# Kernel tuning notes

Measured on AMD Instinct MI355X. Metric: run time of the kernel, lower is better.

The kernel has to match this reference:

```python
import jax, jax.numpy as jnp
import numpy as np

B, T, D = 2, 2048, 2048
H, HKV, RD = 16, 4, 64
DH = D // H          # 128
REP = H // HKV       # 4
NEG = -1e30


def _apply_rope(x, cos, sin, rd):
    # x: (B, h, T, Dh); cos/sin: (T, rd//2) broadcast over (B, h)
    xr, xp = x[..., :rd], x[..., rd:]
    x1, x2 = xr[..., ::2], xr[..., 1::2]
    rot = jnp.stack([x1 * cos - x2 * sin, x1 * sin + x2 * cos], axis=-1)
    rot = rot.reshape(x1.shape[:-1] + (rd,))
    return jnp.concatenate([rot, xp], axis=-1)


def setup_inputs() -> dict:
    key = jax.random.key(0)
    ks = jax.random.split(key, 6)
    x = jax.random.normal(ks[0], (B, T, D), dtype=jnp.float32)
    # rotary tables for the first RD dims (RD//2 frequency pairs)
    inv_freq = 1.0 / (10000.0 ** (np.arange(RD // 2, dtype=np.float32) / (RD // 2)))
    ang = np.arange(T, dtype=np.float32)[:, None] * inv_freq[None, :]  # (T, RD//2)
    cos = jnp.asarray(np.cos(ang), dtype=jnp.float32)
    sin = jnp.asarray(np.sin(ang), dtype=jnp.float32)
    s = 0.02
    Wq = jax.random.normal(ks[1], (H * DH, D), dtype=jnp.float32) * s
    Wk = jax.random.normal(ks[2], (HKV * DH, D), dtype=jnp.float32) * s
    Wv = jax.random.normal(ks[3], (HKV * DH, D), dtype=jnp.float32) * s
    Wo = jax.random.normal(ks[4], (D, D), dtype=jnp.float32) * s
    temp = jnp.full((H,), 1.0 / np.sqrt(DH), dtype=jnp.float32)
    return {"x": x, "cos": cos, "sin": sin, "Wq": Wq, "Wk": Wk, "Wv": Wv, "Wo": Wo, "temp": temp}


def reference(x, cos, sin, Wq, Wk, Wv, Wo, temp):
    Bt, Tt, _ = x.shape
    q = (x @ Wq.T).reshape(Bt, Tt, H, DH).transpose(0, 2, 1, 3)    # (B,H,T,Dh)
    k = (x @ Wk.T).reshape(Bt, Tt, HKV, DH).transpose(0, 2, 1, 3)  # (B,Hkv,T,Dh)
    v = (x @ Wv.T).reshape(Bt, Tt, HKV, DH).transpose(0, 2, 1, 3)
    k = jnp.repeat(k, REP, axis=1)  # GQA repeat_interleave -> (B,H,T,Dh)
    v = jnp.repeat(v, REP, axis=1)
    q = _apply_rope(q, cos, sin, RD)
    k = _apply_rope(k, cos, sin, RD)
    q = q * temp[None, :, None, None]
    # SDPA causal, with default 1/sqrt(Dh) scale on top of learned temp
    scores = jnp.einsum("bhqd,bhkd->bhqk", q, k) / np.sqrt(DH)
    causal = jnp.tril(jnp.ones((Tt, Tt), dtype=bool))
    scores = jnp.where(causal[None, None], scores, NEG)
    attn = jax.nn.softmax(scores, axis=-1)
    out = jnp.einsum("bhqk,bhkd->bhqd", attn, v)  # (B,H,T,Dh)
    out = out.transpose(0, 2, 1, 3).reshape(Bt, Tt, H * DH)
    return out @ Wo.T
```

## Files before the change

### kernel.cpp

```cpp
#include <hip/hip_runtime.h>
#include <hip/hip_bf16.h>
#include <math.h>

#define B_   2
#define T_   2048
#define D_   2048
#define H_   16
#define HKV_ 4
#define DH_  128
#define RD_  64
#define KD_  (HKV_ * DH_)
#define SQKV 3072
#define VOFF 2560

typedef __attribute__((ext_vector_type(8))) short  short8;
typedef __attribute__((ext_vector_type(4))) short  short4v;
typedef __attribute__((ext_vector_type(4))) float  floatx4;

__device__ __forceinline__ void async16(const __hip_bfloat16* g, __hip_bfloat16* l) {
  __builtin_amdgcn_global_load_lds(
      (const __attribute__((address_space(1))) void*)g,
      (__attribute__((address_space(3))) void*)l, 16, 0, 0);
}

__device__ __forceinline__ short bf16b(float x) {
  union { __hip_bfloat16 h; short s; } u;
  u.h = __float2bfloat16(x);
  return u.s;
}

struct ConvArgs {
  const float* src[5];
  __hip_bfloat16* dst[5];
  int n[5];
};

__global__ __launch_bounds__(256) void conv_bf16(ConvArgs a) {
  const int arr = blockIdx.y;
  const int i = (blockIdx.x * 256 + threadIdx.x) * 8;
  if (i >= a.n[arr]) return;
  const float4 f1 = *(const float4*)(a.src[arr] + i);
  const float4 f2 = *(const float4*)(a.src[arr] + i + 4);
  union { short8 v; __hip_bfloat16 h[8]; } o;
  o.h[0] = __float2bfloat16(f1.x); o.h[1] = __float2bfloat16(f1.y);
  o.h[2] = __float2bfloat16(f1.z); o.h[3] = __float2bfloat16(f1.w);
  o.h[4] = __float2bfloat16(f2.x); o.h[5] = __float2bfloat16(f2.y);
  o.h[6] = __float2bfloat16(f2.z); o.h[7] = __float2bfloat16(f2.w);
  *(short8*)(a.dst[arr] + i) = o.v;
}

template <int MODE>
__global__ __launch_bounds__(512, 1) void gemm_192(const __hip_bfloat16* __restrict__ A,
                                                   const __hip_bfloat16* __restrict__ Bw,
                                                   void* __restrict__ Cout,
                                                   __hip_bfloat16* __restrict__ vtout,
                                                   int M, int N, int K, int nwg_x) {
  __shared__ __hip_bfloat16 ABs[3][28 * 512];

  const int tid  = threadIdx.x;
  const int lane = tid & 63;
  const int w    = tid >> 6;
  const int wm   = w >> 2, wn = w & 3;
  const int quad = lane >> 4, m16 = lane & 15;

  const int nwg = gridDim.x;
  const int q8  = nwg >> 3, r8 = nwg & 7;
  const int xcd = blockIdx.x & 7, o8 = blockIdx.x >> 3;
  const int swz = (xcd < r8 ? xcd * (q8 + 1) : r8 * (q8 + 1) + (xcd - r8) * q8) + o8;
  const int bx = swz % nwg_x, by = swz / nwg_x;
  const int bm = by * 256, bn = bx * 192;

  const __hip_bfloat16* gp[4];
  int lp[4];
  if (w < 7) {
#pragma unroll
    for (int e = 0; e < 4; ++e) {
      const int p = w * 4 + e;
      lp[e] = p * 512;
      if (p < 16) gp[e] = A  + (size_t)(bm + p * 16 + m16) * K + quad * 8;
      else        gp[e] = Bw + (size_t)(bn + (p - 16) * 16 + m16) * K + quad * 8;
    }
  }

  const int nt = K >> 5;

  if (w < 7) {
#pragma unroll
    for (int e = 0; e < 4; ++e) async16(gp[e],      &ABs[0][lp[e]]);
#pragma unroll
    for (int e = 0; e < 4; ++e) async16(gp[e] + 32, &ABs[1][lp[e]]);
  }

  floatx4 acc[8][3] = {};
  const int fragoff = (quad * 16 + m16) * 8;

  int cur = 0, stg = 2;
  for (int t = 0; t < nt; ++t) {
    if (t < nt - 1) asm volatile("s_waitcnt vmcnt(4)" ::: "memory");
    else            asm volatile("s_waitcnt vmcnt(0)" ::: "memory");
    __builtin_amdgcn_s_barrier();
    __builtin_amdgcn_sched_barrier(0);

    const __hip_bfloat16* base = &ABs[cur][0];

    short8 a[8], b[3];
#pragma unroll
    for (int i = 0; i < 8; ++i)
      a[i] = *(const short8*)(base + (wm * 8 + i) * 512 + fragoff);
#pragma unroll
    for (int j = 0; j < 3; ++j)
      b[j] = *(const short8*)(base + (16 + wn * 3 + j) * 512 + fragoff);

    if (w < 7 && t + 2 < nt) {
      const size_t ko = (size_t)(t + 2) * 32;
#pragma unroll
      for (int e = 0; e < 4; ++e) async16(gp[e] + ko, &ABs[stg][lp[e]]);
    }
    __builtin_amdgcn_s_setprio(1);
#pragma unroll
    for (int i = 0; i < 8; ++i)
#pragma unroll
      for (int j = 0; j < 3; ++j)
        acc[i][j] = __builtin_amdgcn_mfma_f32_16x16x32_bf16(a[i], b[j], acc[i][j], 0, 0, 0);
    __builtin_amdgcn_s_setprio(0);

    cur = (cur == 2) ? 0 : cur + 1;
    stg = (stg == 2) ? 0 : stg + 1;
  }

#pragma unroll
  for (int mt = 0; mt < 8; ++mt)
#pragma unroll
    for (int j = 0; j < 3; ++j) {
      const int col0 = bn + wn * 48 + j * 16;
      const int row0 = bm + wm * 128 + mt * 16 + quad * 4;
      if (MODE == 2 && col0 >= VOFF) {
        const int dh = col0 + m16 - VOFF;
        const int bb = row0 >> 11, t0 = row0 & (T_ - 1);
        short4v pk;
#pragma unroll
        for (int reg = 0; reg < 4; ++reg) pk[reg] = bf16b(acc[mt][j][reg]);
        *(short4v*)&vtout[((size_t)(bb * HKV_ + (dh >> 7)) * DH_ + (dh & 127)) * T_ + t0] = pk;
      } else {
#pragma unroll
        for (int reg = 0; reg < 4; ++reg) {
          const int row = row0 + reg;
          const int col = col0 + m16;
          if (MODE == 0)
            ((float*)Cout)[(size_t)row * N + col] = acc[mt][j][reg];
          else
            ((__hip_bfloat16*)Cout)[(size_t)row * N + col] = __float2bfloat16(acc[mt][j][reg]);
        }
      }
    }
}

__global__ __launch_bounds__(512, 2) void gemm_k1(const __hip_bfloat16* __restrict__ A,
                                                  const __hip_bfloat16* __restrict__ Bw,
                                                  float* __restrict__ Cout,
                                                  int M, int N, int K, int nwg_x) {
  __shared__ __hip_bfloat16 As[3][8 * 512];
  __shared__ __hip_bfloat16 Bs[3][16 * 512];

  const int tid  = threadIdx.x;
  const int lane = tid & 63;
  const int w    = tid >> 6;
  const int wm   = w >> 2, wn = w & 3;
  const int quad = lane >> 4, m16 = lane & 15;

  const int nwg = gridDim.x;
  const int q8  = nwg >> 3, r8 = nwg & 7;
  const int xcd = blockIdx.x & 7, o8 = blockIdx.x >> 3;
  const int swz = (xcd < r8 ? xcd * (q8 + 1) : r8 * (q8 + 1) + (xcd - r8) * q8) + o8;
  const int bx = swz % nwg_x, by = swz / nwg_x;
  const int bm = by * 128, bn = bx * 256;

  const __hip_bfloat16* gA  = A  + (size_t)(bm + w * 16 + m16) * K + quad * 8;
  const __hip_bfloat16* gB0 = Bw + (size_t)(bn + (w * 2 + 0) * 16 + m16) * K + quad * 8;
  const __hip_bfloat16* gB1 = Bw + (size_t)(bn + (w * 2 + 1) * 16 + m16) * K + quad * 8;

  const int nt = K >> 5;

  async16(gA,       &As[0][w * 512]);
  async16(gB0,      &Bs[0][(w * 2 + 0) * 512]);
  async16(gB1,      &Bs[0][(w * 2 + 1) * 512]);
  async16(gA + 32,  &As[1][w * 512]);
  async16(gB0 + 32, &Bs[1][(w * 2 + 0) * 512]);
  async16(gB1 + 32, &Bs[1][(w * 2 + 1) * 512]);

  floatx4 acc[4][4] = {};
  const int fragoff = (quad * 16 + m16) * 8;

  int cur = 0, stg = 2;
  for (int t = 0; t < nt; ++t) {
    if (t < nt - 1) asm volatile("s_waitcnt vmcnt(3)" ::: "memory");
    else            asm volatile("s_waitcnt vmcnt(0)" ::: "memory");
    __builtin_amdgcn_s_barrier();
    __builtin_amdgcn_sched_barrier(0);

    const __hip_bfloat16* abase = &As[cur][0];
    const __hip_bfloat16* bbase = &Bs[cur][0];

    short8 a[4], b[4];
#pragma unroll
    for (int i = 0; i < 4; ++i) {
      a[i] = *(const short8*)(abase + (wm * 4 + i) * 512 + fragoff);
      b[i] = *(const short8*)(bbase + (wn * 4 + i) * 512 + fragoff);
    }
    if (t + 2 < nt) {
      const size_t ko = (size_t)(t + 2) * 32;
      async16(gA + ko,  &As[stg][w * 512]);
      async16(gB0 + ko, &Bs[stg][(w * 2 + 0) * 512]);
      async16(gB1 + ko, &Bs[stg][(w * 2 + 1) * 512]);
    }
    __builtin_amdgcn_s_setprio(1);
#pragma unroll
    for (int i = 0; i < 4; ++i)
#pragma unroll
      for (int j = 0; j < 4; ++j)
        acc[i][j] = __builtin_amdgcn_mfma_f32_16x16x32_bf16(a[i], b[j], acc[i][j], 0, 0, 0);
    __builtin_amdgcn_s_setprio(0);

    cur = (cur == 2) ? 0 : cur + 1;
    stg = (stg == 2) ? 0 : stg + 1;
  }

#pragma unroll
  for (int mi = 0; mi < 4; ++mi)
#pragma unroll
    for (int nj = 0; nj < 4; ++nj)
#pragma unroll
      for (int reg = 0; reg < 4; ++reg) {
        const int row = bm + wm * 64 + mi * 16 + quad * 4 + reg;
        const int col = bn + wn * 64 + nj * 16 + m16;
        Cout[(size_t)row * N + col] = acc[mi][nj][reg];
      }
}

__global__ __launch_bounds__(256) void rope_qk(__hip_bfloat16* __restrict__ qkv,
                                               const float* __restrict__ cosT,
                                               const float* __restrict__ sinT,
                                               const float* __restrict__ temp,
                                               float inv_sqrt_dh) {
  const int unit = blockIdx.x * 4 + (threadIdx.x >> 6);
  const int lane = threadIdx.x & 63;
  const int M = B_ * T_;
  int bt, off;
  float scale;
  if (unit < M * H_) {
    const int h = unit % H_;
    bt = unit / H_;
    off = h * DH_;
    scale = temp[h] * inv_sqrt_dh;
  } else {
    const int u2 = unit - M * H_;
    const int h = u2 % HKV_;
    bt = u2 / HKV_;
    off = D_ + h * DH_;
    scale = 1.0f;
  }
  const int t = bt & (T_ - 1);
  __hip_bfloat16* p = qkv + (size_t)bt * SQKV + off;
  if (lane < 32) {
    const float x1 = __bfloat162float(p[2 * lane]);
    const float x2 = __bfloat162float(p[2 * lane + 1]);
    const float c = cosT[t * (RD_ / 2) + lane];
    const float s = sinT[t * (RD_ / 2) + lane];
    p[2 * lane]     = __float2bfloat16((x1 * c - x2 * s) * scale);
    p[2 * lane + 1] = __float2bfloat16((x1 * s + x2 * c) * scale);
  } else {
    const int d0 = RD_ + (lane - 32) * 2;
    p[d0]     = __float2bfloat16(__bfloat162float(p[d0]) * scale);
    p[d0 + 1] = __float2bfloat16(__bfloat162float(p[d0 + 1]) * scale);
  }
}

__global__ __launch_bounds__(512, 2) void flash_attn_t2(
    const __hip_bfloat16* __restrict__ qkv,
    const __hip_bfloat16* __restrict__ vt,
    __hip_bfloat16* __restrict__ ao) {
  __shared__ __hip_bfloat16 KV[2][16384];

  const int tid = threadIdx.x, lane = tid & 63, w = tid >> 6;
  const int quad = lane >> 4, m16 = lane & 15;

  const int bid = blockIdx.x;
  const int g = bid & 7;
  const int b = g >> 2, kvh = g & 3;
  const int u = bid >> 3;
  const int qt = 63 - u;
  const int hw = w & 3;
  const int khalf = w >> 2;
  const int h = kvh * 4 + hw;
  const int qRow0 = qt * 32;
  const int ktEnd = (qt >> 1) + 1;

  const size_t bT = (size_t)b * T_;

  short8 qa[2][4];
#pragma unroll
  for (int qi = 0; qi < 2; qi++) {
    const __hip_bfloat16* qp = qkv + (bT + qRow0 + qi * 16 + m16) * SQKV + h * DH_;
#pragma unroll
    for (int ks = 0; ks < 4; ks++) qa[qi][ks] = *(const short8*)(qp + ks * 32 + quad * 8);
  }

  const short one = (short)0x3F80;
  const short4v ones4 = {one, one, one, one};

  const __hip_bfloat16* kptr[2];
  const __hip_bfloat16* vptr[2];
#pragma unroll
  for (int e = 0; e < 2; e++) {
    const int I = w * 2 + e;
    const int panelK = I >> 2, kcK = (I & 3) * 4 + quad;
    kptr[e] = qkv + D_ + (bT + panelK * 16 + m16) * SQKV + kvh * DH_ + kcK * 8;
    const int panelV = I >> 1, tc = (I & 1) * 4 + quad;
    vptr[e] = vt + ((size_t)(b * HKV_ + kvh) * DH_ + panelV * 16 + m16) * T_ + tc * 8;
  }

#pragma unroll
  for (int e = 0; e < 2; e++) {
    const int I = w * 2 + e;
    async16(kptr[e], &KV[0][I * 512]);
    async16(vptr[e], &KV[0][8192 + I * 512]);
    kptr[e] += (size_t)64 * SQKV;
    vptr[e] += 64;
  }

  floatx4 ot[8][2] = {};
  floatx4 lt[2] = {};

  for (int kt = 0; kt < ktEnd; kt++) {
    const int cur = kt & 1;
    __syncthreads();
    if (kt + 1 < ktEnd) {
      const int nxt = cur ^ 1;
#pragma unroll
      for (int e = 0; e < 2; e++) {
        const int I = w * 2 + e;
        async16(kptr[e], &KV[nxt][I * 512]);
        async16(vptr[e], &KV[nxt][8192 + I * 512]);
        kptr[e] += (size_t)64 * SQKV;
        vptr[e] += 64;
      }
    }

    const bool last = (kt == ktEnd - 1);
    if (last && khalf == 1 && ((qt & 1) == 0)) continue;

    floatx4 st[2][2] = {};
#pragma unroll
    for (int ki = 0; ki < 2; ki++) {
      const int kg = khalf * 2 + ki;
#pragma unroll
      for (int ks = 0; ks < 4; ks++) {
        const int unit = kg * 256 + (ks * 4 + quad) * 16 + m16;
        const short8 kf = *(const short8*)&KV[cur][unit * 8];
#pragma unroll
        for (int qi = 0; qi < 2; qi++)
          st[ki][qi] = __builtin_amdgcn_mfma_f32_16x16x32_bf16(kf, qa[qi][ks],
                                                               st[ki][qi], 0, 0, 0);
      }
    }

    if (last && khalf == (qt & 1)) {
#pragma unroll
      for (int ki = 0; ki < 2; ki++)
#pragma unroll
        for (int qi = 0; qi < 2; qi++) {
          const int rowg = qRow0 + qi * 16 + m16;
#pragma unroll
          for (int reg = 0; reg < 4; reg++) {
            const int keyg = kt * 64 + khalf * 32 + ki * 16 + quad * 4 + reg;
            if (keyg > rowg) st[ki][qi][reg] = -1e30f;
          }
        }
    }

    short4v pf[2][2];
#pragma unroll
    for (int ki = 0; ki < 2; ki++)
#pragma unroll
      for (int qi = 0; qi < 2; qi++) {
        short4v t;
#pragma unroll
        for (int reg = 0; reg < 4; reg++) t[reg] = bf16b(__expf(st[ki][qi][reg]));
        pf[ki][qi] = t;
      }

#pragma unroll
    for (int mi = 0; mi < 8; mi++)
#pragma unroll
      for (int ki = 0; ki < 2; ki++) {
        const int kg = khalf * 2 + ki;
        const int unit = mi * 128 + (kg * 2 + (quad >> 1)) * 16 + m16;
        const short4v vf = *(const short4v*)&KV[cur][8192 + unit * 8 + (quad & 1) * 4];
#pragma unroll
        for (int qi = 0; qi < 2; qi++)
          ot[mi][qi] = __builtin_amdgcn_mfma_f32_16x16x16bf16_1k(vf, pf[ki][qi],
                                                                 ot[mi][qi], 0, 0, 0);
      }
#pragma unroll
    for (int ki = 0; ki < 2; ki++)
#pragma unroll
      for (int qi = 0; qi < 2; qi++)
        lt[qi] = __builtin_amdgcn_mfma_f32_16x16x16bf16_1k(ones4, pf[ki][qi],
                                                           lt[qi], 0, 0, 0);
  }

  floatx4* scr = (floatx4*)&KV[0][0];
  __syncthreads();
  if (khalf == 1) {
#pragma unroll
    for (int mi = 0; mi < 6; mi++)
#pragma unroll
      for (int qi = 0; qi < 2; qi++)
        scr[((hw * 6 + mi) * 2 + qi) * 64 + lane] = ot[mi][qi];
  }
  __syncthreads();
  if (khalf == 0) {
#pragma unroll
    for (int mi = 0; mi < 6; mi++)
#pragma unroll
      for (int qi = 0; qi < 2; qi++)
        ot[mi][qi] += scr[((hw * 6 + mi) * 2 + qi) * 64 + lane];
  }
  __syncthreads();
  if (khalf == 1) {
#pragma unroll
    for (int j = 0; j < 2; j++)
#pragma unroll
      for (int qi = 0; qi < 2; qi++)
        scr[((hw * 2 + j) * 2 + qi) * 64 + lane] = ot[6 + j][qi];
#pragma unroll
    for (int qi = 0; qi < 2; qi++)
      scr[1024 + (hw * 2 + qi) * 64 + lane] = lt[qi];
  }
  __syncthreads();
  if (khalf == 0) {
#pragma unroll
    for (int j = 0; j < 2; j++)
#pragma unroll
      for (int qi = 0; qi < 2; qi++)
        ot[6 + j][qi] += scr[((hw * 2 + j) * 2 + qi) * 64 + lane];
#pragma unroll
    for (int qi = 0; qi < 2; qi++)
      lt[qi] += scr[1024 + (hw * 2 + qi) * 64 + lane];

#pragma unroll
    for (int qi = 0; qi < 2; qi++) {
      const float inv = 1.0f / lt[qi][0];
      const size_t gr = (bT + qRow0 + qi * 16 + m16) * D_ + h * DH_;
#pragma unroll
      for (int mi = 0; mi < 8; mi++) {
        short4v o;
#pragma unroll
        for (int reg = 0; reg < 4; reg++) o[reg] = bf16b(ot[mi][qi][reg] * inv);
        *(short4v*)&ao[gr + mi * 16 + quad * 4] = o;
      }
    }
  }
}

extern "C" void kernel_launch(void* const* d_in, const int* in_sizes, int n_in,
                              void* d_out, int out_size, void* d_ws, size_t ws_size,
                              hipStream_t stream) {
  const float* x    = (const float*)d_in[0];
  const float* cosT = (const float*)d_in[1];
  const float* sinT = (const float*)d_in[2];
  const float* Wq   = (const float*)d_in[3];
  const float* Wk   = (const float*)d_in[4];
  const float* Wv   = (const float*)d_in[5];
  const float* Wo   = (const float*)d_in[6];
  const float* temp = (const float*)d_in[7];
  float* out = (float*)d_out;

  const int M = B_ * T_;
  const size_t XN   = (size_t)M * D_;
  const size_t WQN  = (size_t)D_ * D_;
  const size_t WKN  = (size_t)KD_ * D_;
  const size_t QKVN = (size_t)M * SQKV;
  const size_t KN   = (size_t)M * KD_;

  __hip_bfloat16* ws = (__hip_bfloat16*)d_ws;
  __hip_bfloat16* xb    = ws;  ws += XN;
  __hip_bfloat16* wqkvb = ws;  ws += WQN + 2 * WKN;
  __hip_bfloat16* wob   = ws;  ws += WQN;
  __hip_bfloat16* qkvb  = ws;  ws += QKVN;
  __hip_bfloat16* vtb   = ws;  ws += KN;
  __hip_bfloat16* aob   = ws;  ws += XN;

  dim3 blk(256);

  ConvArgs ca;
  ca.src[0] = x;  ca.dst[0] = xb;                  ca.n[0] = (int)XN;
  ca.src[1] = Wq; ca.dst[1] = wqkvb;               ca.n[1] = (int)WQN;
  ca.src[2] = Wk; ca.dst[2] = wqkvb + WQN;         ca.n[2] = (int)WKN;
  ca.src[3] = Wv; ca.dst[3] = wqkvb + WQN + WKN;   ca.n[3] = (int)WKN;
  ca.src[4] = Wo; ca.dst[4] = wob;                 ca.n[4] = (int)WQN;
  conv_bf16<<<dim3(4096, 5), blk, 0, stream>>>(ca);

  gemm_192<2><<<dim3((SQKV / 192) * (M / 256)), dim3(512), 0, stream>>>(
      xb, wqkvb, qkvb, vtb, M, SQKV, D_, SQKV / 192);

  const float inv_sqrt_dh = 1.0f / sqrtf((float)DH_);
  rope_qk<<<(M * (H_ + HKV_)) / 4, blk, 0, stream>>>(qkvb, cosT, sinT, temp, inv_sqrt_dh);

  flash_attn_t2<<<512, dim3(512), 0, stream>>>(qkvb, vtb, aob);

  gemm_k1<<<dim3((D_ / 256) * (M / 128)), dim3(512), 0, stream>>>(
      aob, wob, out, M, D_, D_, D_ / 256);
}
```

Baseline: 305.2 us.

## Split GEMM k-step into two barrier-phased halves and use 16x16x32 MFMA for PV

The GEMM main loop is split into two halves, each loading four A fragments, issuing half of the async global-to-LDS stage loads, and running its MFMAs between extra workgroup barriers. This interleaves memory traffic with compute and lowers register pressure from A fragments. In attention, the P fragments are rearranged across lanes with shuffles into 8-wide operands, so the PV product and the row-sum use the larger 16x16x32 bf16 MFMA with one 16-byte V read per tile instead of two 16x16x16 ops. The risk is the added barriers and shuffle overhead, plus correctness depending on the V layout in LDS matching the new indexing.

```diff
diff --git a/kernel.cpp b/kernel.cpp
--- a/kernel.cpp
+++ b/kernel.cpp
@@ -27,6 +27,14 @@
   union { __hip_bfloat16 h; short s; } u;
   u.h = __float2bfloat16(x);
   return u.s;
+}
+
+__device__ __forceinline__ short4v shfl4(short4v v, int src) {
+  union { short4v v; int i[2]; } a, r;
+  a.v = v;
+  r.i[0] = __shfl(a.i[0], src, 64);
+  r.i[1] = __shfl(a.i[1], src, 64);
+  return r.v;
 }
 
 struct ConvArgs {
@@ -102,26 +110,48 @@
     __builtin_amdgcn_sched_barrier(0);
 
     const __hip_bfloat16* base = &ABs[cur][0];
-
-    short8 a[8], b[3];
-#pragma unroll
-    for (int i = 0; i < 8; ++i)
-      a[i] = *(const short8*)(base + (wm * 8 + i) * 512 + fragoff);
+    const bool doStage = (w < 7) && (t + 2 < nt);
+    const size_t ko = (size_t)(t + 2) * 32;
+
+    short8 a0[4], b[3];
+#pragma unroll
+    for (int i = 0; i < 4; ++i)
+      a0[i] = *(const short8*)(base + (wm * 8 + i) * 512 + fragoff);
 #pragma unroll
     for (int j = 0; j < 3; ++j)
       b[j] = *(const short8*)(base + (16 + wn * 3 + j) * 512 + fragoff);
-
-    if (w < 7 && t + 2 < nt) {
-      const size_t ko = (size_t)(t + 2) * 32;
-#pragma unroll
-      for (int e = 0; e < 4; ++e) async16(gp[e] + ko, &ABs[stg][lp[e]]);
-    }
+    if (doStage) {
+      async16(gp[0] + ko, &ABs[stg][lp[0]]);
+      async16(gp[1] + ko, &ABs[stg][lp[1]]);
+    }
+    __builtin_amdgcn_s_barrier();
+    __builtin_amdgcn_sched_barrier(0);
     __builtin_amdgcn_s_setprio(1);
 #pragma unroll
-    for (int i = 0; i < 8; ++i)
+    for (int i = 0; i < 4; ++i)
 #pragma unroll
       for (int j = 0; j < 3; ++j)
-        acc[i][j] = __builtin_amdgcn_mfma_f32_16x16x32_bf16(a[i], b[j], acc[i][j], 0, 0, 0);
+        acc[i][j] = __builtin_amdgcn_mfma_f32_16x16x32_bf16(a0[i], b[j], acc[i][j], 0, 0, 0);
+    __builtin_amdgcn_s_setprio(0);
+    __builtin_amdgcn_s_barrier();
+    __builtin_amdgcn_sched_barrier(0);
+
+    short8 a1[4];
+#pragma unroll
+    for (int i = 0; i < 4; ++i)
+      a1[i] = *(const short8*)(base + (wm * 8 + 4 + i) * 512 + fragoff);
+    if (doStage) {
+      async16(gp[2] + ko, &ABs[stg][lp[2]]);
+      async16(gp[3] + ko, &ABs[stg][lp[3]]);
+    }
+    __builtin_amdgcn_s_barrier();
+    __builtin_amdgcn_sched_barrier(0);
+    __builtin_amdgcn_s_setprio(1);
+#pragma unroll
+    for (int i = 0; i < 4; ++i)
+#pragma unroll
+      for (int j = 0; j < 3; ++j)
+        acc[4 + i][j] = __builtin_amdgcn_mfma_f32_16x16x32_bf16(a1[i], b[j], acc[4 + i][j], 0, 0, 0);
     __builtin_amdgcn_s_setprio(0);
 
     cur = (cur == 2) ? 0 : cur + 1;
@@ -306,7 +336,7 @@
   }
 
   const short one = (short)0x3F80;
-  const short4v ones4 = {one, one, one, one};
+  const short8 ones8 = {one, one, one, one, one, one, one, one};
 
   const __hip_bfloat16* kptr[2];
   const __hip_bfloat16* vptr[2];
@@ -330,6 +360,9 @@
 
   floatx4 ot[8][2] = {};
   floatx4 lt[2] = {};
+
+  const int srcLo = (((quad * 2) & 3) << 4) | m16;
+  const int srcHi = (((quad * 2 + 1) & 3) << 4) | m16;
 
   for (int kt = 0; kt < ktEnd; kt++) {
     const int cur = kt & 1;
@@ -389,24 +422,30 @@
         pf[ki][qi] = t;
       }
 
-#pragma unroll
-    for (int mi = 0; mi < 8; mi++)
-#pragma unroll
-      for (int ki = 0; ki < 2; ki++) {
-        const int kg = khalf * 2 + ki;
-        const int unit = mi * 128 + (kg * 2 + (quad >> 1)) * 16 + m16;
-        const short4v vf = *(const short4v*)&KV[cur][8192 + unit * 8 + (quad & 1) * 4];
-#pragma unroll
-        for (int qi = 0; qi < 2; qi++)
-          ot[mi][qi] = __builtin_amdgcn_mfma_f32_16x16x16bf16_1k(vf, pf[ki][qi],
-                                                                 ot[mi][qi], 0, 0, 0);
-      }
-#pragma unroll
-    for (int ki = 0; ki < 2; ki++)
+    short8 p8[2];
+#pragma unroll
+    for (int qi = 0; qi < 2; qi++) {
+      const short4v l0 = shfl4(pf[0][qi], srcLo);
+      const short4v l1 = shfl4(pf[1][qi], srcLo);
+      const short4v h0 = shfl4(pf[0][qi], srcHi);
+      const short4v h1 = shfl4(pf[1][qi], srcHi);
+      const short4v lo = (quad & 2) ? l1 : l0;
+      const short4v hi = (quad & 2) ? h1 : h0;
+      p8[qi] = (short8){lo[0], lo[1], lo[2], lo[3], hi[0], hi[1], hi[2], hi[3]};
+    }
+
+#pragma unroll
+    for (int mi = 0; mi < 8; mi++) {
+      const short8 vf = *(const short8*)&KV[cur][8192 + (mi * 2 + khalf) * 512 +
+                                                 (quad * 16 + m16) * 8];
 #pragma unroll
       for (int qi = 0; qi < 2; qi++)
-        lt[qi] = __builtin_amdgcn_mfma_f32_16x16x16bf16_1k(ones4, pf[ki][qi],
-                                                           lt[qi], 0, 0, 0);
+        ot[mi][qi] = __builtin_amdgcn_mfma_f32_16x16x32_bf16(vf, p8[qi],
+                                                             ot[mi][qi], 0, 0, 0);
+    }
+#pragma unroll
+    for (int qi = 0; qi < 2; qi++)
+      lt[qi] = __builtin_amdgcn_mfma_f32_16x16x32_bf16(ones8, p8[qi], lt[qi], 0, 0, 0);
   }
 
   floatx4* scr = (floatx4*)&KV[0][0];
```

New measurement: 305.0 us. No clear change (-0.1%).

## Switch GEMM to double-buffered LDS with two-phase ping-pong and 2 blocks/CU

Applied to the files above, without the earlier changes.

Reduces the GEMM LDS staging from triple to double buffering, which allows two 512-thread workgroups per CU (launch bounds changed to 2). Each K-step is split into two halves. Each half loads part of the A fragments and issues half of the next tile's async loads, and extra barriers separate the halves so waves interleave compute and memory. The aim is more concurrency and latency hiding through occupancy. The cost is a shallower prefetch (vmcnt(0) every step), many more barriers, and tighter register pressure.

```diff
diff --git a/kernel.cpp b/kernel.cpp
--- a/kernel.cpp
+++ b/kernel.cpp
@@ -50,12 +50,12 @@
 }
 
 template <int MODE>
-__global__ __launch_bounds__(512, 1) void gemm_192(const __hip_bfloat16* __restrict__ A,
+__global__ __launch_bounds__(512, 2) void gemm_192(const __hip_bfloat16* __restrict__ A,
                                                    const __hip_bfloat16* __restrict__ Bw,
                                                    void* __restrict__ Cout,
                                                    __hip_bfloat16* __restrict__ vtout,
                                                    int M, int N, int K, int nwg_x) {
-  __shared__ __hip_bfloat16 ABs[3][28 * 512];
+  __shared__ __hip_bfloat16 ABs[2][28 * 512];
 
   const int tid  = threadIdx.x;
   const int lane = tid & 63;
@@ -86,46 +86,62 @@
 
   if (w < 7) {
 #pragma unroll
-    for (int e = 0; e < 4; ++e) async16(gp[e],      &ABs[0][lp[e]]);
-#pragma unroll
-    for (int e = 0; e < 4; ++e) async16(gp[e] + 32, &ABs[1][lp[e]]);
+    for (int e = 0; e < 4; ++e) async16(gp[e], &ABs[0][lp[e]]);
   }
 
   floatx4 acc[8][3] = {};
   const int fragoff = (quad * 16 + m16) * 8;
 
-  int cur = 0, stg = 2;
   for (int t = 0; t < nt; ++t) {
-    if (t < nt - 1) asm volatile("s_waitcnt vmcnt(4)" ::: "memory");
-    else            asm volatile("s_waitcnt vmcnt(0)" ::: "memory");
+    const int cur = t & 1, stg = cur ^ 1;
+    asm volatile("s_waitcnt vmcnt(0)" ::: "memory");
     __builtin_amdgcn_s_barrier();
     __builtin_amdgcn_sched_barrier(0);
 
     const __hip_bfloat16* base = &ABs[cur][0];
-
-    short8 a[8], b[3];
-#pragma unroll
-    for (int i = 0; i < 8; ++i)
-      a[i] = *(const short8*)(base + (wm * 8 + i) * 512 + fragoff);
+    const bool doStage = (w < 7) && (t + 1 < nt);
+    const size_t ko = (size_t)(t + 1) * 32;
+
+    short8 a0[4], b[3];
+#pragma unroll
+    for (int i = 0; i < 4; ++i)
+      a0[i] = *(const short8*)(base + (wm * 8 + i) * 512 + fragoff);
 #pragma unroll
     for (int j = 0; j < 3; ++j)
       b[j] = *(const short8*)(base + (16 + wn * 3 + j) * 512 + fragoff);
-
-    if (w < 7 && t + 2 < nt) {
-      const size_t ko = (size_t)(t + 2) * 32;
-#pragma unroll
-      for (int e = 0; e < 4; ++e) async16(gp[e] + ko, &ABs[stg][lp[e]]);
-    }
+    if (doStage) {
+      async16(gp[0] + ko, &ABs[stg][lp[0]]);
+      async16(gp[1] + ko, &ABs[stg][lp[1]]);
+    }
+    __builtin_amdgcn_s_barrier();
+    __builtin_amdgcn_sched_barrier(0);
     __builtin_amdgcn_s_setprio(1);
 #pragma unroll
-    for (int i = 0; i < 8; ++i)
+    for (int i = 0; i < 4; ++i)
 #pragma unroll
       for (int j = 0; j < 3; ++j)
-        acc[i][j] = __builtin_amdgcn_mfma_f32_16x16x32_bf16(a[i], b[j], acc[i][j], 0, 0, 0);
+        acc[i][j] = __builtin_amdgcn_mfma_f32_16x16x32_bf16(a0[i], b[j], acc[i][j], 0, 0, 0);
     __builtin_amdgcn_s_setprio(0);
-
-    cur = (cur == 2) ? 0 : cur + 1;
-    stg = (stg == 2) ? 0 : stg + 1;
+    __builtin_amdgcn_s_barrier();
+    __builtin_amdgcn_sched_barrier(0);
+
+    short8 a1[4];
+#pragma unroll
+    for (int i = 0; i < 4; ++i)
+      a1[i] = *(const short8*)(base + (wm * 8 + 4 + i) * 512 + fragoff);
+    if (doStage) {
+      async16(gp[2] + ko, &ABs[stg][lp[2]]);
+      async16(gp[3] + ko, &ABs[stg][lp[3]]);
+    }
+    __builtin_amdgcn_s_barrier();
+    __builtin_amdgcn_sched_barrier(0);
+    __builtin_amdgcn_s_setprio(1);
+#pragma unroll
+    for (int i = 0; i < 4; ++i)
+#pragma unroll
+      for (int j = 0; j < 3; ++j)
+        acc[4 + i][j] = __builtin_amdgcn_mfma_f32_16x16x32_bf16(a1[i], b[j], acc[4 + i][j], 0, 0, 0);
+    __builtin_amdgcn_s_setprio(0);
   }
 
 #pragma unroll
```

Result: slower. 327.1 us (+7.2%).
